# Kernel optimization log

Hardware: AMD Instinct MI355X
Metric: run time of the kernel (lower is better)

Reference implementation:

```python
import jax, jax.numpy as jnp
import numpy as np

STEP = 4      # LIF time steps folded into batch dim
TAU = 2.0
THR = 1.0
ALPHA = 4.0   # SigmoidGrad surrogate sharpness
EPS = 1e-5    # BatchNorm eps (eval mode, running_mean=0, running_var=1)

@jax.custom_vjp
def spike(x):
    return (x >= 0.0).astype(x.dtype)

def _spike_fwd(x):
    return spike(x), x

def _spike_bwd(x, g):
    s = jax.nn.sigmoid(ALPHA * x)
    return (g * ALPHA * s * (1.0 - s),)

spike.defvjp(_spike_fwd, _spike_bwd)

def lif(x):
    # x: (T*B, ...). BrainCog LIFNode: mem += (inp - mem)/tau; spike = H(mem - thr); hard reset with detached spike.
    TB = x.shape[0]
    B = TB // STEP
    xt = x.reshape(STEP, B, *x.shape[1:])
    def step(mem, xi):
        mem = mem + (xi - mem) / TAU
        s = spike(mem - THR)
        mem = mem * (1.0 - jax.lax.stop_gradient(s))
        return mem, s
    _, s = jax.lax.scan(step, jnp.zeros_like(xt[0]), xt)
    return s.reshape(x.shape)

_BN_SCALE = 1.0 / np.sqrt(1.0 + EPS)

def bn(x, g, b):
    # eval-mode BN over channel axis 1, running_mean=0, running_var=1
    shp = (1, -1) + (1,) * (x.ndim - 2)
    return x * (g * _BN_SCALE).reshape(shp) + b.reshape(shp)

def _forward(x, res_attn, k_w, v_w, router_w, router_b, router_g, router_be,
             exp_w, exp_g, exp_b, proj_w, proj_b, proj_g, proj_be,
             fc1_w, fc1_b, fc1_g, fc1_be, dw_w, dw_b, dw_g, dw_be,
             fc2_w, fc2_b, fc2_g, fc2_be):
    TB, C, H, W = x.shape
    xs = x.reshape(TB, C, H * W)                     # (TB, C, N)
    # SSA (mode='base': d = dim)
    k = lif(jnp.einsum('od,bdn->bon', k_w, xs))      # (TB, ed, N)
    v = lif(jnp.einsum('od,bdn->bon', v_w, xs))      # (TB, C, N)
    w = lif(bn(jnp.einsum('ed,bdn->ben', router_w, xs) + router_b[None, :, None],
               router_g, router_be))                 # (TB, E, N) soft routing weights (spikes)
    # all experts computed (soft routing) -> vectorize over expert axis e
    q = jnp.einsum('eod,bdn->ebon', exp_w, xs)       # (E, TB, ed, N)
    q = q * (exp_g * _BN_SCALE)[:, None, :, None] + exp_b[:, None, :, None]
    q = jax.vmap(lif)(q)
    attn = jnp.einsum('ebcn,bcm->ebnm', q, k)        # q^T @ k : (E, TB, N, N)
    res = jnp.einsum('ebnm,bdm->ebnd', attn, v)      # attn @ v^T : (E, TB, N, C)
    res = jax.vmap(lif)(res)
    y = jnp.einsum('ben,ebnd->bdn', w, res)          # router-weighted sum over experts
    y = jnp.einsum('od,bdn->bon', proj_w, y) + proj_b[None, :, None]
    y = lif(bn(y, proj_g, proj_be).reshape(TB, C, H, W))
    x = x + y
    # MLP: fc1 (1x1) -> BN -> LIF -> chunk -> dwconv3x3 -> BN -> LIF -> gate -> fc2 (1x1) -> BN -> LIF
    h = lif(bn(jnp.einsum('oc,bchw->bohw', fc1_w, x) + fc1_b[None, :, None, None], fc1_g, fc1_be))
    x1, x2 = jnp.split(h, 2, axis=1)
    x1 = jax.lax.conv_general_dilated(x1, dw_w, (1, 1), 'SAME',
                                      feature_group_count=x1.shape[1],
                                      dimension_numbers=('NCHW', 'OIHW', 'NCHW')) + dw_b[None, :, None, None]
    x1 = lif(bn(x1, dw_g, dw_be))
    m = x1 * x2
    m = lif(bn(jnp.einsum('oc,bchw->bohw', fc2_w, m) + fc2_b[None, :, None, None], fc2_g, fc2_be))
    return x + m

def setup_inputs() -> dict:
    key = jax.random.key(0)
    ks = jax.random.split(key, 26)
    dim, ed, E, H, W, B = 384, 96, 4, 16, 16, 8
    TB = STEP * B
    hid = dim // 3 * 16   # MLP overrides hidden_features: 2048
    hh = hid // 2
    def nrm(k, shape, std):
        return std * jax.random.normal(k, shape, dtype=jnp.float32)
    return {
        'x': nrm(ks[0], (TB, dim, H, W), 1.0),
        'res_attn': jnp.zeros((1,), jnp.float32),
        'k_w': nrm(ks[1], (ed, dim), 0.05),
        'v_w': nrm(ks[2], (dim, dim), 0.05),
        'router_w': nrm(ks[3], (E, dim), 0.05),
        'router_b': nrm(ks[4], (E,), 0.05),
        'router_g': 1.0 + nrm(ks[5], (E,), 0.1),
        'router_be': nrm(ks[6], (E,), 0.1),
        'exp_w': nrm(ks[7], (E, ed, dim), 0.05),
        'exp_g': 1.0 + nrm(ks[8], (E, ed), 0.1),
        'exp_b': nrm(ks[9], (E, ed), 0.1),
        'proj_w': nrm(ks[10], (dim, dim), 0.05),
        'proj_b': nrm(ks[11], (dim,), 0.05),
        'proj_g': 1.0 + nrm(ks[12], (dim,), 0.1),
        'proj_be': nrm(ks[13], (dim,), 0.1),
        'fc1_w': nrm(ks[14], (hid, dim), 0.05),
        'fc1_b': nrm(ks[15], (hid,), 0.05),
        'fc1_g': 1.0 + nrm(ks[16], (hid,), 0.1),
        'fc1_be': nrm(ks[17], (hid,), 0.1),
        'dw_w': nrm(ks[18], (hh, 1, 3, 3), 0.3),
        'dw_b': nrm(ks[19], (hh,), 0.05),
        'dw_g': 1.0 + nrm(ks[20], (hh,), 0.1),
        'dw_be': nrm(ks[21], (hh,), 0.1),
        'fc2_w': nrm(ks[22], (dim, hh), 0.05),
        'fc2_b': nrm(ks[23], (dim,), 0.05),
        'fc2_g': 1.0 + nrm(ks[24], (dim,), 0.1),
        'fc2_be': nrm(ks[25], (dim,), 0.1),
    }

def reference(x, res_attn, k_w, v_w, router_w, router_b, router_g, router_be,
              exp_w, exp_g, exp_b, proj_w, proj_b, proj_g, proj_be,
              fc1_w, fc1_b, fc1_g, fc1_be, dw_w, dw_b, dw_g, dw_be,
              fc2_w, fc2_b, fc2_g, fc2_be):
    return _forward(x, res_attn, k_w, v_w, router_w, router_b, router_g, router_be,
                    exp_w, exp_g, exp_b, proj_w, proj_b, proj_g, proj_be,
                    fc1_w, fc1_b, fc1_g, fc1_be, dw_w, dw_b, dw_g, dw_be,
                    fc2_w, fc2_b, fc2_g, fc2_be)
```

## Files before the change

### kernel.cpp

```cpp
#include <hip/hip_runtime.h>
#include <cstdint>
#include <cstddef>

namespace {

typedef unsigned short ushort_t;
typedef _Float16 half_t;
typedef __attribute__((ext_vector_type(8))) short bf8v;
typedef __attribute__((ext_vector_type(8))) _Float16 h8v;
typedef __attribute__((ext_vector_type(4))) float f4v;

constexpr float BNS = 0.99999500003749973f;

constexpr int TB = 32;
constexpr int C  = 384;
constexpr int N  = 256;
constexpr int ROWS = 868;
constexpr int HID = 2048;
constexpr int HH  = 1024;

constexpr size_t O_A1S  = 0;
constexpr size_t O_A1B  = 896;
constexpr size_t O_APS  = 1792;
constexpr size_t O_APB  = 2176;
constexpr size_t O_AHS  = 2560;
constexpr size_t O_AHB  = 4608;
constexpr size_t O_ADS  = 6656;
constexpr size_t O_ADB  = 7680;
constexpr size_t O_AFS  = 8704;
constexpr size_t O_AFB  = 9088;
constexpr size_t O_DWT  = 9472;
constexpr size_t O_WPRE0 = 18688;
constexpr size_t O_WPRE1 = 190720;
constexpr size_t O_WPRJ0 = 362752;
constexpr size_t O_WPRJ1 = 436480;
constexpr size_t O_WF10  = 510208;
constexpr size_t O_WF11  = 903424;
constexpr size_t O_WF20  = 1296640;
constexpr size_t O_WF21  = 1493248;
constexpr size_t O_XTPRE = 2023168;
constexpr size_t O_SPKB  = 5168896;
constexpr size_t O_QT    = 8724224;
constexpr size_t O_KT    = 10297088;
constexpr size_t O_ATTNB = 10690304;
constexpr size_t O_RES   = 14884608;
constexpr size_t O_YT    = 1689856;
constexpr size_t O_XF0   = O_QT;
constexpr size_t O_XF1   = O_ATTNB;
constexpr size_t O_H     = O_RES;
constexpr size_t O_M     = 23273216;

__device__ __forceinline__ void gload16(const void* g, void* l)
{
  __builtin_amdgcn_global_load_lds(
      (const __attribute__((address_space(1))) unsigned int*)g,
      (__attribute__((address_space(3))) unsigned int*)l, 16, 0, 0);
}

__global__ __launch_bounds__(256) void affines_all(
    const float* __restrict__ rb, const float* __restrict__ rg, const float* __restrict__ rbe,
    const float* __restrict__ eg, const float* __restrict__ eb,
    const float* __restrict__ pg, const float* __restrict__ pb, const float* __restrict__ pbe,
    const float* __restrict__ hg, const float* __restrict__ hb, const float* __restrict__ hbe,
    const float* __restrict__ dg, const float* __restrict__ db, const float* __restrict__ dbe,
    const float* __restrict__ fg, const float* __restrict__ fb, const float* __restrict__ fbe,
    const float* __restrict__ dw, float* __restrict__ ws)
{
  int u = blockIdx.x * 256 + threadIdx.x;
  if (u < 896) {
    float s, b;
    if (u < 480)      { s = 1.0f; b = 0.0f; }
    else if (u < 484) { int e = u - 480; s = rg[e] * BNS; b = rb[e] * rg[e] * BNS + rbe[e]; }
    else if (u < 868) { int j = u - 484; s = eg[j] * BNS; b = eb[j]; }
    else              { s = 0.0f; b = 0.0f; }
    ws[O_A1S + u] = s; ws[O_A1B + u] = b;
  } else if (u < 1280) {
    int j = u - 896;
    ws[O_APS + j] = pg[j] * BNS; ws[O_APB + j] = pb[j] * pg[j] * BNS + pbe[j];
  } else if (u < 3328) {
    int j = u - 1280;
    ws[O_AHS + j] = hg[j] * BNS; ws[O_AHB + j] = hb[j] * hg[j] * BNS + hbe[j];
  } else if (u < 4352) {
    int j = u - 3328;
    ws[O_ADS + j] = dg[j] * BNS; ws[O_ADB + j] = db[j] * dg[j] * BNS + dbe[j];
  } else if (u < 4736) {
    int j = u - 4352;
    ws[O_AFS + j] = fg[j] * BNS; ws[O_AFB + j] = fb[j] * fg[j] * BNS + fbe[j];
  } else if (u < 4736 + HH * 9) {
    int j = u - 4736; int ch = j / 9, i = j % 9;
    ws[O_DWT + i * HH + ch] = dw[j];
  }
}

__global__ __launch_bounds__(256) void split_all(
    const float* __restrict__ kw, const float* __restrict__ vw,
    const float* __restrict__ rw, const float* __restrict__ ew,
    const float* __restrict__ pw, const float* __restrict__ f1w, const float* __restrict__ f2w,
    float* __restrict__ ws)
{
  int u = blockIdx.x * 256 + threadIdx.x;
  float v; size_t o0, o1; int idx;
  if (u < 344064) {
    int r = u / 384, d = u - r * 384;
    if (r < 96)       v = kw[r * 384 + d];
    else if (r < 480) v = vw[(r - 96) * 384 + d];
    else if (r < 484) v = rw[(r - 480) * 384 + d];
    else if (r < 868) v = ew[(r - 484) * 384 + d];
    else              v = 0.0f;
    o0 = O_WPRE0; o1 = O_WPRE1; idx = u;
  } else if (u < 491520) {
    idx = u - 344064; v = pw[idx]; o0 = O_WPRJ0; o1 = O_WPRJ1;
  } else if (u < 1277952) {
    idx = u - 491520; v = f1w[idx]; o0 = O_WF10; o1 = O_WF11;
  } else if (u < 1671168) {
    idx = u - 1277952; v = f2w[idx]; o0 = O_WF20; o1 = O_WF21;
  } else return;
  half_t h0 = (half_t)v;
  half_t h1 = (half_t)(v - (float)h0);
  ((half_t*)(ws + o0))[idx] = h0;
  ((half_t*)(ws + o1))[idx] = h1;
}

__global__ __launch_bounds__(256) void split_xt(
    const float* __restrict__ X, half_t* __restrict__ X0, half_t* __restrict__ X1, int D)
{
  __shared__ float tile[32][33];
  int tb = blockIdx.z, n0 = blockIdx.x * 32, d0 = blockIdx.y * 32;
  const float* src = X + (size_t)tb * D * N;
  int t = threadIdx.x;
  int nn = t & 31, ds = t >> 5;
#pragma unroll
  for (int l = 0; l < 4; ++l) {
    int dd = ds + 8 * l;
    tile[dd][nn] = src[(size_t)(d0 + dd) * N + n0 + nn];
  }
  __syncthreads();
  int dd2 = t & 31, ns = t >> 5;
#pragma unroll
  for (int l = 0; l < 4; ++l) {
    int nn2 = ns + 8 * l;
    float v = tile[dd2][nn2];
    half_t h0 = (half_t)v;
    half_t h1 = (half_t)(v - (float)h0);
    size_t o = ((size_t)tb * N + n0 + nn2) * D + d0 + dd2;
    X0[o] = h0; X1[o] = h1;
  }
}

template<int NPROD, int MODE>
__global__ __launch_bounds__(256, 3) void sgemm_lif(
    const half_t* __restrict__ X0, const half_t* __restrict__ X1,
    const half_t* __restrict__ W0, const half_t* __restrict__ W1,
    const float* __restrict__ aS, const float* __restrict__ aB,
    const float* __restrict__ xin, void* __restrict__ dst,
    int O, int D)
{
  constexpr int XHALF = (NPROD == 3) ? 8192 : 4096;
  __shared__ half_t smem[2 * (XHALF + 4096)];
  half_t* xb0 = smem;
  half_t* xb1 = smem + XHALF;
  half_t* wb0 = smem + 2 * XHALF;
  half_t* wb1 = smem + 2 * XHALF + 4096;

  int b = blockIdx.z;
  int nblk = blockIdx.x * 32, o0 = blockIdx.y * 64;
  int tid = threadIdx.x, w = tid >> 6, l = tid & 63;
  int lr = l & 15, lk = l >> 4;
  int wn = w & 1, wo = w >> 1;

  auto STAGE = [&](int kt, int bi) {
    half_t* xb = bi ? xb1 : xb0;
    half_t* wb = bi ? wb1 : wb0;
    constexpr int XISS = (NPROD == 3) ? 4 : 2;
#pragma unroll
    for (int j = 0; j < XISS; ++j) {
      int gi = w * (XISS * 64) + j * 64 + l;
      int s = gi & 7, n = (gi >> 3) & 31, tz = gi >> 8;
      int g = s ^ (n & 7);
      int lk2 = g & 3;
      const half_t* src; int tt;
      if (NPROD == 3) { tt = tz; src = (g >> 2) ? X1 : X0; }
      else            { tt = tz * 2 + (g >> 2); src = X0; }
      const half_t* gp = src + ((size_t)((tt * 8 + b) * 256 + nblk + n)) * D + kt + lk2 * 8;
      gload16(gp, xb + (size_t)(w * (XISS * 64) + j * 64) * 8);
    }
#pragma unroll
    for (int j = 0; j < 2; ++j) {
      int gi = w * 128 + j * 64 + l;
      int s = gi & 7, ol = gi >> 3;
      int g = s ^ (ol & 7);
      const half_t* src = (g >> 2) ? W1 : W0;
      const half_t* gp = src + (size_t)(o0 + ol) * D + kt + (g & 3) * 8;
      gload16(gp, wb + (size_t)(w * 128 + j * 64) * 8);
    }
  };

  f4v acc[4][2] = {};
  STAGE(0, 0);
  __syncthreads();
  int buf = 0;
  for (int kt = 0; kt < D; kt += 32) {
    if (kt + 32 < D) STAGE(kt + 32, buf ^ 1);
    half_t* xb = buf ? xb1 : xb0;
    half_t* wb = buf ? wb1 : wb0;
    h8v bb[2][2];
#pragma unroll
    for (int ct = 0; ct < 2; ++ct)
#pragma unroll
      for (int op = 0; op < 2; ++op) {
        int ol = wo * 32 + ct * 16 + lr;
        bb[ct][op] = *(const h8v*)(wb + ol * 64 + (((op << 2) | lk) ^ (ol & 7)) * 8);
      }
    h8v a[4][2];
    int nl = wn * 16 + lr;
#pragma unroll
    for (int tt = 0; tt < 4; ++tt)
#pragma unroll
      for (int op = 0; op < (NPROD == 3 ? 2 : 1); ++op) {
        int row = (NPROD == 3) ? (tt * 32 + nl) : ((tt >> 1) * 32 + nl);
        int g = (NPROD == 3) ? ((op << 2) | lk) : (((tt & 1) << 2) | lk);
        a[tt][op] = *(const h8v*)(xb + row * 64 + (g ^ (nl & 7)) * 8);
      }
#pragma unroll
    for (int tt = 0; tt < 4; ++tt)
#pragma unroll
      for (int ct = 0; ct < 2; ++ct) {
        acc[tt][ct] = __builtin_amdgcn_mfma_f32_16x16x32_f16(a[tt][0], bb[ct][0], acc[tt][ct], 0, 0, 0);
        acc[tt][ct] = __builtin_amdgcn_mfma_f32_16x16x32_f16(a[tt][0], bb[ct][1], acc[tt][ct], 0, 0, 0);
        if (NPROD == 3)
          acc[tt][ct] = __builtin_amdgcn_mfma_f32_16x16x32_f16(a[tt][1], bb[ct][0], acc[tt][ct], 0, 0, 0);
      }
    __syncthreads();
    buf ^= 1;
  }

  unsigned sb_[2];
#pragma unroll
  for (int ct = 0; ct < 2; ++ct) {
    int o = o0 + wo * 32 + ct * 16 + lr;
    float s = aS[o], bbv = aB[o];
    unsigned bits = 0;
#pragma unroll
    for (int r = 0; r < 4; ++r) {
      float mem = 0.0f;
#pragma unroll
      for (int tt = 0; tt < 4; ++tt) {
        float z = acc[tt][ct][r] * s + bbv;
        mem += (z - mem) * 0.5f;
        if (mem >= 1.0f) { bits |= 1u << (r * 4 + tt); mem = 0.0f; }
      }
    }
    sb_[ct] = bits;
  }

  ushort_t* lsu = (ushort_t*)smem;
  float*    lsf = (float*)smem;
  for (int tt = 0; tt < 4; ++tt) {
    __syncthreads();
#pragma unroll
    for (int ct = 0; ct < 2; ++ct) {
      int ol = wo * 32 + ct * 16 + lr;
#pragma unroll
      for (int r = 0; r < 4; ++r) {
        int nl2 = wn * 16 + lk * 4 + r;
        bool fire = (sb_[ct] >> (r * 4 + tt)) & 1;
        if (MODE == 0)      lsu[ol * 40 + nl2] = fire ? (ushort_t)0x3F80 : (ushort_t)0;
        else if (MODE == 2) lsu[nl2 * 80 + ol] = fire ? (ushort_t)0x3C00 : (ushort_t)0;
        else                lsf[ol * 40 + nl2] = fire ? 1.0f : 0.0f;
      }
    }
    __syncthreads();
    int tb = tt * 8 + b;
    if (MODE == 0) {
      int row = tid >> 2, cb = (tid & 3) * 8;
      if (o0 + row < O) {
        ushort_t* dp = (ushort_t*)dst + ((size_t)tb * 868 + o0 + row) * 256 + nblk + cb;
        *(uint4*)dp = *(uint4*)&lsu[row * 40 + cb];
      }
    } else if (MODE == 2) {
      int row = tid >> 3, cb = (tid & 7) * 8;
      half_t* dp = (half_t*)dst + ((size_t)tb * 256 + nblk + row) * (size_t)O + o0 + cb;
      *(uint4*)dp = *(uint4*)&lsu[row * 80 + cb];
    } else if (MODE == 1) {
      int row = tid >> 2, cb = (tid & 3) * 8;
      float* op = (float*)dst + ((size_t)tb * O + o0 + row) * 256 + nblk + cb;
      const float* xp = xin + ((size_t)tb * O + o0 + row) * 256 + nblk + cb;
#pragma unroll
      for (int j = 0; j < 2; ++j) {
        float4 sv = *(float4*)&lsf[row * 40 + cb + j * 4];
        float4 xv = *(const float4*)(xp + j * 4);
        float4 ov = {xv.x + sv.x, xv.y + sv.y, xv.z + sv.z, xv.w + sv.w};
        *(float4*)(op + j * 4) = ov;
      }
    } else {
      int row = tid >> 2, cb = (tid & 3) * 8;
      float* op = (float*)dst + ((size_t)tb * O + o0 + row) * 256 + nblk + cb;
#pragma unroll
      for (int j = 0; j < 2; ++j) {
        float4 sv = *(float4*)&lsf[row * 40 + cb + j * 4];
        float4 ov = *(float4*)(op + j * 4);
        ov.x += sv.x; ov.y += sv.y; ov.z += sv.z; ov.w += sv.w;
        *(float4*)(op + j * 4) = ov;
      }
    }
  }
}

__global__ __launch_bounds__(256) void transpose_spk(
    const ushort_t* __restrict__ SPKB, ushort_t* __restrict__ dst, int srcBase)
{
  __shared__ ushort_t tile[32][33];
  int z = blockIdx.z, tb = z & 31, ey = z >> 5;
  const ushort_t* src = SPKB + ((size_t)tb * ROWS + srcBase + ey * 96) * N;
  ushort_t* d = dst + (size_t)z * N * 96;
  int n0 = blockIdx.x * 32, c0 = blockIdx.y * 32;
  int t = threadIdx.x, nn = t & 31, cs = t >> 5;
#pragma unroll
  for (int l = 0; l < 4; ++l) {
    int cc = cs + 8 * l;
    tile[cc][nn] = src[(size_t)(c0 + cc) * N + n0 + nn];
  }
  __syncthreads();
  int cc2 = t & 31, ns = t >> 5;
#pragma unroll
  for (int l = 0; l < 4; ++l) {
    int nn2 = ns + 8 * l;
    d[(size_t)(n0 + nn2) * 96 + c0 + cc2] = tile[cc2][nn2];
  }
}

__global__ __launch_bounds__(256) void attn_mfma(
    const ushort_t* __restrict__ QT, const ushort_t* __restrict__ KT, ushort_t* __restrict__ ATTNB)
{
  int bi = blockIdx.y, tb = bi & 31;
  const ushort_t* q  = QT + (size_t)bi * N * 96;
  const ushort_t* kk = KT + (size_t)tb * N * 96;
  ushort_t* ob = ATTNB + (size_t)bi * N * N;
  int m0 = blockIdx.x * 128;
  int t = threadIdx.x, w = t >> 6, l = t & 63;
  int lr = l & 15, lk = l >> 4;
  int nb = w * 64;
  f4v acc[4][8] = {};
  for (int kt = 0; kt < 96; kt += 32) {
    bf8v a[4], b[8];
#pragma unroll
    for (int rt = 0; rt < 4; ++rt)
      a[rt] = *reinterpret_cast<const bf8v*>(q + (size_t)(nb + rt * 16 + lr) * 96 + kt + lk * 8);
#pragma unroll
    for (int ct = 0; ct < 8; ++ct)
      b[ct] = *reinterpret_cast<const bf8v*>(kk + (size_t)(m0 + ct * 16 + lr) * 96 + kt + lk * 8);
#pragma unroll
    for (int rt = 0; rt < 4; ++rt)
#pragma unroll
      for (int ct = 0; ct < 8; ++ct)
        acc[rt][ct] = __builtin_amdgcn_mfma_f32_16x16x32_bf16(a[rt], b[ct], acc[rt][ct], 0, 0, 0);
  }
#pragma unroll
  for (int rt = 0; rt < 4; ++rt)
#pragma unroll
    for (int ct = 0; ct < 8; ++ct)
#pragma unroll
      for (int r = 0; r < 4; ++r) {
        int n = nb + rt * 16 + lk * 4 + r;
        int m = m0 + ct * 16 + lr;
        float v = acc[rt][ct][r];
        ob[(size_t)n * N + m] = (ushort_t)(__builtin_bit_cast(unsigned, v) >> 16);
      }
}

__global__ __launch_bounds__(256) void res_mfma(
    const ushort_t* __restrict__ ATTNB, const ushort_t* __restrict__ SPKB, float* __restrict__ RES)
{
  int bi = blockIdx.y, tb = bi & 31;
  const ushort_t* A = ATTNB + (size_t)bi * N * N;
  const ushort_t* V = SPKB + ((size_t)tb * ROWS + 96) * N;
  float* ob = RES + (size_t)bi * N * C;
  int d0 = blockIdx.x * 96;
  int t = threadIdx.x, w = t >> 6, l = t & 63;
  int lr = l & 15, lk = l >> 4;
  int nb = w * 64;
  f4v acc[4][6] = {};
  for (int kt = 0; kt < 256; kt += 32) {
    bf8v a[4], b[6];
#pragma unroll
    for (int rt = 0; rt < 4; ++rt)
      a[rt] = *reinterpret_cast<const bf8v*>(A + (size_t)(nb + rt * 16 + lr) * N + kt + lk * 8);
#pragma unroll
    for (int ct = 0; ct < 6; ++ct)
      b[ct] = *reinterpret_cast<const bf8v*>(V + (size_t)(d0 + ct * 16 + lr) * N + kt + lk * 8);
#pragma unroll
    for (int rt = 0; rt < 4; ++rt)
#pragma unroll
      for (int ct = 0; ct < 6; ++ct)
        acc[rt][ct] = __builtin_amdgcn_mfma_f32_16x16x32_bf16(a[rt], b[ct], acc[rt][ct], 0, 0, 0);
  }
#pragma unroll
  for (int rt = 0; rt < 4; ++rt)
#pragma unroll
    for (int ct = 0; ct < 6; ++ct)
#pragma unroll
      for (int r = 0; r < 4; ++r) {
        int n = nb + rt * 16 + lk * 4 + r;
        int d = d0 + ct * 16 + lr;
        ob[(size_t)n * C + d] = acc[rt][ct][r];
      }
}

__global__ __launch_bounds__(128) void y_lif(
    const ushort_t* __restrict__ SPKB, const float* __restrict__ RES, half_t* __restrict__ YT)
{
  int d = blockIdx.x * 128 + threadIdx.x;
  int n = blockIdx.y, b = blockIdx.z;
  float v[4] = {0.0f, 0.0f, 0.0f, 0.0f};
#pragma unroll
  for (int e = 0; e < 4; ++e) {
    float mem = 0.0f;
#pragma unroll
    for (int t = 0; t < 4; ++t) {
      float r = RES[(((size_t)(e * 32 + t * 8 + b) * 256) + n) * 384 + d];
      mem += (r - mem) * 0.5f;
      if (mem >= 1.0f) {
        mem = 0.0f;
        ushort_t wu = SPKB[((size_t)(t * 8 + b) * ROWS + 480 + e) * 256 + n];
        if (wu) v[t] += 1.0f;
      }
    }
  }
#pragma unroll
  for (int t = 0; t < 4; ++t)
    YT[((size_t)(t * 8 + b) * 256 + n) * 384 + d] = (half_t)v[t];
}

__global__ __launch_bounds__(256) void dwconv_nhwc(
    const half_t* __restrict__ H, const float* __restrict__ DWT,
    const float* __restrict__ aS, const float* __restrict__ aB, half_t* __restrict__ M)
{
  int u = blockIdx.x * 256 + threadIdx.x;
  int ch = u & 1023;
  int n = (u >> 10) & 255;
  int b = u >> 18;
  int px = n & 15, py = n >> 4;
  float w[9];
#pragma unroll
  for (int i = 0; i < 9; ++i) w[i] = DWT[i * HH + ch];
  float s = aS[ch], bb = aB[ch];
  float mem = 0.0f;
#pragma unroll
  for (int t = 0; t < 4; ++t) {
    size_t base = (size_t)(t * 8 + b) * 256;
    float acc = 0.0f;
#pragma unroll
    for (int dy = 0; dy < 3; ++dy) {
      int yy = py + dy - 1;
      if (yy < 0 || yy > 15) continue;
#pragma unroll
      for (int dx = 0; dx < 3; ++dx) {
        int xx = px + dx - 1;
        if (xx < 0 || xx > 15) continue;
        acc += (float)H[(base + yy * 16 + xx) * HID + ch] * w[dy * 3 + dx];
      }
    }
    float z = acc * s + bb;
    mem += (z - mem) * 0.5f;
    float sp = (mem >= 1.0f) ? 1.0f : 0.0f;
    mem = (sp != 0.0f) ? 0.0f : mem;
    float x2 = (float)H[(base + n) * HID + HH + ch];
    M[(base + n) * HH + ch] = (half_t)(sp * x2);
  }
}

}

extern "C" void kernel_launch(void* const* d_in, const int* in_sizes, int n_in,
                              void* d_out, int out_size, void* d_ws, size_t ws_size,
                              hipStream_t stream)
{
  const float* x         = (const float*)d_in[0];
  const float* k_w       = (const float*)d_in[2];
  const float* v_w       = (const float*)d_in[3];
  const float* router_w  = (const float*)d_in[4];
  const float* router_b  = (const float*)d_in[5];
  const float* router_g  = (const float*)d_in[6];
  const float* router_be = (const float*)d_in[7];
  const float* exp_w     = (const float*)d_in[8];
  const float* exp_g     = (const float*)d_in[9];
  const float* exp_b     = (const float*)d_in[10];
  const float* proj_w    = (const float*)d_in[11];
  const float* proj_b    = (const float*)d_in[12];
  const float* proj_g    = (const float*)d_in[13];
  const float* proj_be   = (const float*)d_in[14];
  const float* fc1_w     = (const float*)d_in[15];
  const float* fc1_b     = (const float*)d_in[16];
  const float* fc1_g     = (const float*)d_in[17];
  const float* fc1_be    = (const float*)d_in[18];
  const float* dw_w      = (const float*)d_in[19];
  const float* dw_b      = (const float*)d_in[20];
  const float* dw_g      = (const float*)d_in[21];
  const float* dw_be     = (const float*)d_in[22];
  const float* fc2_w     = (const float*)d_in[23];
  const float* fc2_b     = (const float*)d_in[24];
  const float* fc2_g     = (const float*)d_in[25];
  const float* fc2_be    = (const float*)d_in[26];

  float* ws  = (float*)d_ws;
  float* out = (float*)d_out;
  ushort_t* spkb = (ushort_t*)(ws + O_SPKB);
  ushort_t* qt   = (ushort_t*)(ws + O_QT);
  ushort_t* ktb  = (ushort_t*)(ws + O_KT);
  ushort_t* attb = (ushort_t*)(ws + O_ATTNB);
  half_t* wpre0 = (half_t*)(ws + O_WPRE0), *wpre1 = (half_t*)(ws + O_WPRE1);
  half_t* wprj0 = (half_t*)(ws + O_WPRJ0), *wprj1 = (half_t*)(ws + O_WPRJ1);
  half_t* wf10  = (half_t*)(ws + O_WF10),  *wf11  = (half_t*)(ws + O_WF11);
  half_t* wf20  = (half_t*)(ws + O_WF20),  *wf21  = (half_t*)(ws + O_WF21);
  half_t* xtpre0 = (half_t*)(ws + O_XTPRE), *xtpre1 = xtpre0 + (size_t)TB * N * C;
  half_t* yt    = (half_t*)(ws + O_YT);
  half_t* xf0   = (half_t*)(ws + O_XF0), *xf1 = (half_t*)(ws + O_XF1);
  half_t* hbuf  = (half_t*)(ws + O_H);
  half_t* mbuf  = (half_t*)(ws + O_M);
  dim3 blk(256);

  affines_all<<<55, blk, 0, stream>>>(router_b, router_g, router_be, exp_g, exp_b,
                                      proj_g, proj_b, proj_be, fc1_g, fc1_b, fc1_be,
                                      dw_g, dw_b, dw_be, fc2_g, fc2_b, fc2_be, dw_w, ws);
  split_all<<<6528, blk, 0, stream>>>(k_w, v_w, router_w, exp_w, proj_w, fc1_w, fc2_w, ws);

  split_xt<<<dim3(8, 12, 32), blk, 0, stream>>>(x, xtpre0, xtpre1, C);
  sgemm_lif<3, 0><<<dim3(8, 14, 8), blk, 0, stream>>>(
      xtpre0, xtpre1, wpre0, wpre1, ws + O_A1S, ws + O_A1B, nullptr, spkb, 868, C);

  transpose_spk<<<dim3(8, 3, 32),  blk, 0, stream>>>(spkb, ktb, 0);
  transpose_spk<<<dim3(8, 3, 128), blk, 0, stream>>>(spkb, qt, 484);
  attn_mfma<<<dim3(2, 128), blk, 0, stream>>>(qt, ktb, attb);
  res_mfma<<<dim3(4, 128), blk, 0, stream>>>(attb, spkb, ws + O_RES);
  y_lif<<<dim3(3, 256, 8), dim3(128), 0, stream>>>(spkb, ws + O_RES, yt);

  sgemm_lif<2, 1><<<dim3(8, 6, 8), blk, 0, stream>>>(
      yt, nullptr, wprj0, wprj1, ws + O_APS, ws + O_APB, x, out, 384, C);

  split_xt<<<dim3(8, 12, 32), blk, 0, stream>>>(out, xf0, xf1, C);
  sgemm_lif<3, 2><<<dim3(8, 32, 8), blk, 0, stream>>>(
      xf0, xf1, wf10, wf11, ws + O_AHS, ws + O_AHB, nullptr, hbuf, 2048, C);

  dwconv_nhwc<<<dim3(8192), blk, 0, stream>>>(hbuf, ws + O_DWT, ws + O_ADS, ws + O_ADB, mbuf);

  sgemm_lif<2, 3><<<dim3(8, 6, 8), blk, 0, stream>>>(
      mbuf, nullptr, wf20, wf21, ws + O_AFS, ws + O_AFB, nullptr, out, 384, HH);
}
```

Before: 353.4 us.

## Fuse res GEMM with y-LIF and fold fp16 split into proj epilogue

Replaces the separate res_mfma and y_lif kernels with one res_y kernel. It computes attn@v per tile for all four time steps, runs the LIF and router gating in registers, and writes the summed expert spikes directly as fp16. This removes the large fp32 RES intermediate and its round trip through global memory. The proj sgemm epilogue now also emits the hi/lo fp16 split of its output via an LDS transpose, which removes a separate split_xt launch. The cost is smaller per-block MFMA tiles with less operand reuse in res_y, and extra syncs and LDS traffic in the proj epilogue.

```diff
diff --git a/kernel.cpp b/kernel.cpp
--- a/kernel.cpp
+++ b/kernel.cpp
@@ -8,6 +8,7 @@
 typedef _Float16 half_t;
 typedef __attribute__((ext_vector_type(8))) short bf8v;
 typedef __attribute__((ext_vector_type(8))) _Float16 h8v;
+typedef __attribute__((ext_vector_type(4))) _Float16 h4v;
 typedef __attribute__((ext_vector_type(4))) float f4v;
 
 constexpr float BNS = 0.99999500003749973f;
@@ -43,11 +44,10 @@
 constexpr size_t O_QT    = 8724224;
 constexpr size_t O_KT    = 10297088;
 constexpr size_t O_ATTNB = 10690304;
-constexpr size_t O_RES   = 14884608;
 constexpr size_t O_YT    = 1689856;
 constexpr size_t O_XF0   = O_QT;
 constexpr size_t O_XF1   = O_ATTNB;
-constexpr size_t O_H     = O_RES;
+constexpr size_t O_H     = 14884608;
 constexpr size_t O_M     = 23273216;
 
 __device__ __forceinline__ void gload16(const void* g, void* l)
@@ -153,6 +153,7 @@
     const half_t* __restrict__ W0, const half_t* __restrict__ W1,
     const float* __restrict__ aS, const float* __restrict__ aB,
     const float* __restrict__ xin, void* __restrict__ dst,
+    half_t* __restrict__ xo0, half_t* __restrict__ xo1,
     int O, int D)
 {
   constexpr int XHALF = (NPROD == 3) ? 8192 : 4096;
@@ -255,6 +256,7 @@
 
   ushort_t* lsu = (ushort_t*)smem;
   float*    lsf = (float*)smem;
+  float*    lsx = (float*)smem + 64 * 40;
   for (int tt = 0; tt < 4; ++tt) {
     __syncthreads();
 #pragma unroll
@@ -291,7 +293,24 @@
         float4 xv = *(const float4*)(xp + j * 4);
         float4 ov = {xv.x + sv.x, xv.y + sv.y, xv.z + sv.z, xv.w + sv.w};
         *(float4*)(op + j * 4) = ov;
-      }
+        lsx[(cb + j * 4 + 0) * 68 + row] = ov.x;
+        lsx[(cb + j * 4 + 1) * 68 + row] = ov.y;
+        lsx[(cb + j * 4 + 2) * 68 + row] = ov.z;
+        lsx[(cb + j * 4 + 3) * 68 + row] = ov.w;
+      }
+      __syncthreads();
+      int rn = tid >> 3, co = (tid & 7) * 8;
+      h8v h0, h1;
+#pragma unroll
+      for (int j = 0; j < 8; ++j) {
+        float v = lsx[rn * 68 + co + j];
+        half_t a0 = (half_t)v;
+        h0[j] = a0;
+        h1[j] = (half_t)(v - (float)a0);
+      }
+      size_t xo = ((size_t)tb * 256 + nblk + rn) * 384 + o0 + co;
+      *(h8v*)(xo0 + xo) = h0;
+      *(h8v*)(xo1 + xo) = h1;
     } else {
       int row = tid >> 2, cb = (tid & 3) * 8;
       float* op = (float*)dst + ((size_t)tb * O + o0 + row) * 256 + nblk + cb;
@@ -368,67 +387,85 @@
       }
 }
 
-__global__ __launch_bounds__(256) void res_mfma(
-    const ushort_t* __restrict__ ATTNB, const ushort_t* __restrict__ SPKB, float* __restrict__ RES)
-{
-  int bi = blockIdx.y, tb = bi & 31;
-  const ushort_t* A = ATTNB + (size_t)bi * N * N;
-  const ushort_t* V = SPKB + ((size_t)tb * ROWS + 96) * N;
-  float* ob = RES + (size_t)bi * N * C;
-  int d0 = blockIdx.x * 96;
-  int t = threadIdx.x, w = t >> 6, l = t & 63;
+__global__ __launch_bounds__(256) void res_y(
+    const ushort_t* __restrict__ ATTNB, const ushort_t* __restrict__ SPKB,
+    half_t* __restrict__ YT)
+{
+  __shared__ ushort_t wlds[512];
+  __shared__ half_t wt[4][32][36];
+  int b = blockIdx.z;
+  int n0 = blockIdx.y * 32;
+  int d0 = blockIdx.x * 32;
+  int tid = threadIdx.x, e = tid >> 6, l = tid & 63;
   int lr = l & 15, lk = l >> 4;
-  int nb = w * 64;
-  f4v acc[4][6] = {};
-  for (int kt = 0; kt < 256; kt += 32) {
-    bf8v a[4], b[6];
-#pragma unroll
-    for (int rt = 0; rt < 4; ++rt)
-      a[rt] = *reinterpret_cast<const bf8v*>(A + (size_t)(nb + rt * 16 + lr) * N + kt + lk * 8);
-#pragma unroll
-    for (int ct = 0; ct < 6; ++ct)
-      b[ct] = *reinterpret_cast<const bf8v*>(V + (size_t)(d0 + ct * 16 + lr) * N + kt + lk * 8);
-#pragma unroll
-    for (int rt = 0; rt < 4; ++rt)
-#pragma unroll
-      for (int ct = 0; ct < 6; ++ct)
-        acc[rt][ct] = __builtin_amdgcn_mfma_f32_16x16x32_bf16(a[rt], b[ct], acc[rt][ct], 0, 0, 0);
-  }
-#pragma unroll
-  for (int rt = 0; rt < 4; ++rt)
-#pragma unroll
-    for (int ct = 0; ct < 6; ++ct)
+  for (int j = tid; j < 512; j += 256) {
+    int ee = j >> 7, t = (j >> 5) & 3, nl = j & 31;
+    wlds[j] = SPKB[((size_t)((t * 8 + b) * ROWS) + 480 + ee) * 256 + n0 + nl];
+  }
+  __syncthreads();
+  f4v acc[4][2][2] = {};
+#pragma unroll
+  for (int t = 0; t < 4; ++t) {
+    const ushort_t* A = ATTNB + (size_t)(e * 32 + t * 8 + b) * 65536;
+    const ushort_t* V = SPKB + ((size_t)((t * 8 + b) * ROWS) + 96) * 256;
+#pragma unroll
+    for (int kt = 0; kt < 256; kt += 32) {
+      bf8v a[2], bb[2];
+#pragma unroll
+      for (int rt = 0; rt < 2; ++rt)
+        a[rt] = *(const bf8v*)(A + (size_t)(n0 + rt * 16 + lr) * 256 + kt + lk * 8);
+#pragma unroll
+      for (int ct = 0; ct < 2; ++ct)
+        bb[ct] = *(const bf8v*)(V + (size_t)(d0 + ct * 16 + lr) * 256 + kt + lk * 8);
+#pragma unroll
+      for (int rt = 0; rt < 2; ++rt)
+#pragma unroll
+        for (int ct = 0; ct < 2; ++ct)
+          acc[t][rt][ct] = __builtin_amdgcn_mfma_f32_16x16x32_bf16(a[rt], bb[ct], acc[t][rt][ct], 0, 0, 0);
+    }
+  }
+  unsigned sb2[2][2] = {{0, 0}, {0, 0}};
+#pragma unroll
+  for (int rt = 0; rt < 2; ++rt)
+#pragma unroll
+    for (int ct = 0; ct < 2; ++ct)
 #pragma unroll
       for (int r = 0; r < 4; ++r) {
-        int n = nb + rt * 16 + lk * 4 + r;
-        int d = d0 + ct * 16 + lr;
-        ob[(size_t)n * C + d] = acc[rt][ct][r];
-      }
-}
-
-__global__ __launch_bounds__(128) void y_lif(
-    const ushort_t* __restrict__ SPKB, const float* __restrict__ RES, half_t* __restrict__ YT)
-{
-  int d = blockIdx.x * 128 + threadIdx.x;
-  int n = blockIdx.y, b = blockIdx.z;
-  float v[4] = {0.0f, 0.0f, 0.0f, 0.0f};
-#pragma unroll
-  for (int e = 0; e < 4; ++e) {
-    float mem = 0.0f;
-#pragma unroll
-    for (int t = 0; t < 4; ++t) {
-      float r = RES[(((size_t)(e * 32 + t * 8 + b) * 256) + n) * 384 + d];
-      mem += (r - mem) * 0.5f;
-      if (mem >= 1.0f) {
-        mem = 0.0f;
-        ushort_t wu = SPKB[((size_t)(t * 8 + b) * ROWS + 480 + e) * 256 + n];
-        if (wu) v[t] += 1.0f;
-      }
-    }
-  }
-#pragma unroll
-  for (int t = 0; t < 4; ++t)
-    YT[((size_t)(t * 8 + b) * 256 + n) * 384 + d] = (half_t)v[t];
+        int nl = rt * 16 + lk * 4 + r;
+        float mem = 0.0f;
+#pragma unroll
+        for (int t = 0; t < 4; ++t) {
+          float v = acc[t][rt][ct][r];
+          mem += (v - mem) * 0.5f;
+          if (mem >= 1.0f) {
+            mem = 0.0f;
+            if (wlds[(e * 4 + t) * 32 + nl]) sb2[rt][ct] |= 1u << (t * 4 + r);
+          }
+        }
+      }
+  for (int t = 0; t < 4; ++t) {
+    __syncthreads();
+#pragma unroll
+    for (int rt = 0; rt < 2; ++rt)
+#pragma unroll
+      for (int ct = 0; ct < 2; ++ct)
+#pragma unroll
+        for (int r = 0; r < 4; ++r) {
+          int nl = rt * 16 + lk * 4 + r;
+          int dl = ct * 16 + lr;
+          wt[e][nl][dl] = ((sb2[rt][ct] >> (t * 4 + r)) & 1) ? (half_t)1.0f : (half_t)0.0f;
+        }
+    __syncthreads();
+    int row = tid >> 3, cb = (tid & 7) * 4;
+    h4v o4;
+#pragma unroll
+    for (int j = 0; j < 4; ++j) {
+      float s = (float)wt[0][row][cb + j] + (float)wt[1][row][cb + j]
+              + (float)wt[2][row][cb + j] + (float)wt[3][row][cb + j];
+      o4[j] = (half_t)s;
+    }
+    *(h4v*)(YT + ((size_t)((t * 8 + b) * 256) + n0 + row) * 384 + d0 + cb) = o4;
+  }
 }
 
 __global__ __launch_bounds__(256) void dwconv_nhwc(
@@ -526,23 +563,24 @@
 
   split_xt<<<dim3(8, 12, 32), blk, 0, stream>>>(x, xtpre0, xtpre1, C);
   sgemm_lif<3, 0><<<dim3(8, 14, 8), blk, 0, stream>>>(
-      xtpre0, xtpre1, wpre0, wpre1, ws + O_A1S, ws + O_A1B, nullptr, spkb, 868, C);
+      xtpre0, xtpre1, wpre0, wpre1, ws + O_A1S, ws + O_A1B, nullptr, spkb,
+      nullptr, nullptr, 868, C);
 
   transpose_spk<<<dim3(8, 3, 32),  blk, 0, stream>>>(spkb, ktb, 0);
   transpose_spk<<<dim3(8, 3, 128), blk, 0, stream>>>(spkb, qt, 484);
   attn_mfma<<<dim3(2, 128), blk, 0, stream>>>(qt, ktb, attb);
-  res_mfma<<<dim3(4, 128), blk, 0, stream>>>(attb, spkb, ws + O_RES);
-  y_lif<<<dim3(3, 256, 8), dim3(128), 0, stream>>>(spkb, ws + O_RES, yt);
+  res_y<<<dim3(12, 8, 8), blk, 0, stream>>>(attb, spkb, yt);
 
   sgemm_lif<2, 1><<<dim3(8, 6, 8), blk, 0, stream>>>(
-      yt, nullptr, wprj0, wprj1, ws + O_APS, ws + O_APB, x, out, 384, C);
-
-  split_xt<<<dim3(8, 12, 32), blk, 0, stream>>>(out, xf0, xf1, C);
+      yt, nullptr, wprj0, wprj1, ws + O_APS, ws + O_APB, x, out, xf0, xf1, 384, C);
+
   sgemm_lif<3, 2><<<dim3(8, 32, 8), blk, 0, stream>>>(
-      xf0, xf1, wf10, wf11, ws + O_AHS, ws + O_AHB, nullptr, hbuf, 2048, C);
+      xf0, xf1, wf10, wf11, ws + O_AHS, ws + O_AHB, nullptr, hbuf,
+      nullptr, nullptr, 2048, C);
 
   dwconv_nhwc<<<dim3(8192), blk, 0, stream>>>(hbuf, ws + O_DWT, ws + O_ADS, ws + O_ADB, mbuf);
 
   sgemm_lif<2, 3><<<dim3(8, 6, 8), blk, 0, stream>>>(
-      mbuf, nullptr, wf20, wf21, ws + O_AFS, ws + O_AFB, nullptr, out, 384, HH);
-}
+      mbuf, nullptr, wf20, wf21, ws + O_AFS, ws + O_AFB, nullptr, out,
+      nullptr, nullptr, 384, HH);
+}
```

New measurement: 348.5 us. No clear change (-1.4%).
